# Performance work log

Hardware: AMD Instinct MI355X
Metric: run time of the kernel (lower is better)

## Reference

```python
import jax, jax.numpy as jnp
import numpy as np

D_MODEL = 1024
N_HEADS = 16
D_HEAD = 64
INIT_RANGE = 0.02
IGNORE = -100000.0


def setup_inputs() -> dict:
    key = jax.random.key(0)
    ks = jax.random.split(key, 5)
    x = jax.random.normal(ks[0], (2, 2048, D_MODEL), dtype=jnp.float32)
    W_Q = jax.random.normal(ks[1], (N_HEADS, D_MODEL, D_HEAD), dtype=jnp.float32) * INIT_RANGE
    W_K = jax.random.normal(ks[2], (N_HEADS, D_MODEL, D_HEAD), dtype=jnp.float32) * INIT_RANGE
    W_V = jax.random.normal(ks[3], (N_HEADS, D_MODEL, D_HEAD), dtype=jnp.float32) * INIT_RANGE
    W_O = jax.random.normal(ks[4], (N_HEADS, D_HEAD, D_MODEL), dtype=jnp.float32) * INIT_RANGE
    b_Q = jnp.zeros((N_HEADS, D_HEAD), dtype=jnp.float32)
    b_K = jnp.zeros((N_HEADS, D_HEAD), dtype=jnp.float32)
    b_V = jnp.zeros((N_HEADS, D_HEAD), dtype=jnp.float32)
    b_O = jnp.zeros((D_MODEL,), dtype=jnp.float32)
    return {"normalized_resid_pre": x, "W_Q": W_Q, "W_K": W_K, "W_V": W_V,
            "W_O": W_O, "b_Q": b_Q, "b_K": b_K, "b_V": b_V, "b_O": b_O}


def reference(normalized_resid_pre, W_Q, W_K, W_V, W_O, b_Q, b_K, b_V, b_O):
    x = normalized_resid_pre  # [b, s, d_model]
    q = jnp.einsum('bsd,hde->bshe', x, W_Q) + b_Q  # [b, s, h, d_head]
    k = jnp.einsum('bsd,hde->bshe', x, W_K) + b_K
    v = jnp.einsum('bsd,hde->bshe', x, W_V) + b_V
    scores = jnp.einsum('bqhe,bkhe->bhqk', q, k) / jnp.sqrt(jnp.float32(D_HEAD))
    s = x.shape[1]
    causal = jnp.arange(s)[:, None] >= jnp.arange(s)[None, :]  # [q, k]
    scores = jnp.where(causal, scores, jnp.float32(IGNORE))
    pattern = jax.nn.softmax(scores, axis=-1)  # [b, h, q, k]
    z = jnp.einsum('bkhe,bhqk->bqhe', v, pattern)
    out = jnp.einsum('bqhe,hed->bqd', z, W_O) + b_O
    return out
```

## Files before the change

kernel.cpp:

```cpp
#include <hip/hip_runtime.h>

#define SEQ 2048
#define BATCH 2
#define DM 1024
#define NH 16
#define DH 64

typedef __bf16 bf16;
typedef __bf16 bf16x8 __attribute__((ext_vector_type(8)));
typedef __bf16 bf16x4 __attribute__((ext_vector_type(4)));
typedef float f32x4 __attribute__((ext_vector_type(4)));

#define MFMA16(a, b, c) __builtin_amdgcn_mfma_f32_16x16x32_bf16((a), (b), (c), 0, 0, 0)

#if __has_builtin(__builtin_amdgcn_exp2f)
#define EXP2(x) __builtin_amdgcn_exp2f(x)
#else
#define EXP2(x) exp2f(x)
#endif

#define QSCALE 0.18033688f

typedef __attribute__((address_space(3))) void lds_void;
typedef __attribute__((address_space(1))) void glb_void;
__device__ __forceinline__ void gld16(void* lds, const void* g) {
    __builtin_amdgcn_global_load_lds((const glb_void*)g, (lds_void*)lds, 16, 0, 0);
}

__global__ __launch_bounds__(256) void k_prep(const float* __restrict__ x,
                                              const float* __restrict__ WQ,
                                              const float* __restrict__ WK,
                                              const float* __restrict__ WV,
                                              const float* __restrict__ WO,
                                              bf16* __restrict__ xb,
                                              bf16* __restrict__ wT,
                                              bf16* __restrict__ woT) {
    int bx = blockIdx.x;
    int t = threadIdx.x;
    if (bx < 2048) {
        int g = bx * 256 + t;
        const float4* x4 = (const float4*)x;
        float4 a = x4[2 * g];
        float4 b = x4[2 * g + 1];
        bf16x8 o;
        o[0] = (bf16)a.x; o[1] = (bf16)a.y; o[2] = (bf16)a.z; o[3] = (bf16)a.w;
        o[4] = (bf16)b.x; o[5] = (bf16)b.y; o[6] = (bf16)b.z; o[7] = (bf16)b.w;
        *(bf16x8*)(xb + 8 * g) = o;
        return;
    }
    __shared__ bf16 T[64 * 65];
    if (bx < 2816) {
        int id = bx - 2048;
        int kt = id & 15, ph = id >> 4;
        int p = ph >> 4, h = ph & 15;
        const float* Wp = (p == 0) ? WQ : (p == 1) ? WK : WV;
        const float* src = Wp + ((size_t)h * DM + (size_t)kt * 64) * DH;
        for (int i = 0; i < 4; i++) {
            int c = t + 256 * i;
            int r = c >> 4;
            int col = (c & 15) * 4;
            float4 v = *(const float4*)&src[r * 64 + col];
            T[(col + 0) * 65 + r] = (bf16)v.x;
            T[(col + 1) * 65 + r] = (bf16)v.y;
            T[(col + 2) * 65 + r] = (bf16)v.z;
            T[(col + 3) * 65 + r] = (bf16)v.w;
        }
        __syncthreads();
        bf16* dst = wT + (size_t)ph * 64 * DM + (size_t)kt * 64;
        for (int i = 0; i < 2; i++) {
            int c = t + 256 * i;
            int e = c >> 3;
            int k0 = (c & 7) * 8;
            bf16x8 o;
            for (int j = 0; j < 8; j++) o[j] = T[e * 65 + k0 + j];
            *(bf16x8*)&dst[(size_t)e * DM + k0] = o;
        }
    } else {
        int id = bx - 2816;
        int ht = id & 15, dt = id >> 4;
        for (int i = 0; i < 4; i++) {
            int c = t + 256 * i;
            int r = c >> 4;
            int col = (c & 15) * 4;
            float4 v = *(const float4*)&WO[((size_t)(ht * 64 + r)) * DM + dt * 64 + col];
            T[(col + 0) * 65 + r] = (bf16)v.x;
            T[(col + 1) * 65 + r] = (bf16)v.y;
            T[(col + 2) * 65 + r] = (bf16)v.z;
            T[(col + 3) * 65 + r] = (bf16)v.w;
        }
        __syncthreads();
        for (int i = 0; i < 2; i++) {
            int c = t + 256 * i;
            int d = c >> 3;
            int h0 = (c & 7) * 8;
            bf16x8 o;
            for (int j = 0; j < 8; j++) o[j] = T[d * 65 + h0 + j];
            *(bf16x8*)&woT[((size_t)(dt * 64 + d)) * DM + ht * 64 + h0] = o;
        }
    }
}

__global__ __launch_bounds__(512, 2) void k_qkv(const bf16* __restrict__ xb,
                                                const bf16* __restrict__ wT,
                                                const float* __restrict__ bQ,
                                                const float* __restrict__ bK,
                                                const float* __restrict__ bV,
                                                bf16* __restrict__ Qb,
                                                bf16* __restrict__ Kb,
                                                bf16* __restrict__ VTf) {
    int mt = blockIdx.x, nt = blockIdx.y;
    __shared__ __align__(16) char sm[114688];
    int t = threadIdx.x;
    int lane = t & 63, w = t >> 6;
    int l15 = lane & 15, quad = lane >> 4;
    int wr = w >> 2, wc = w & 3;
    int m0 = mt * 256;
    int n0 = nt * 192;

    int P0 = t * 16;
    int L0 = P0 ^ (((P0 >> 7) & 3) << 4);
    int row0 = L0 >> 6, kc0 = (L0 >> 4) & 3;
    int P1 = 8192 + t * 16;
    int L1 = P1 ^ (((P1 >> 7) & 3) << 4);
    int row1 = L1 >> 6, kc1 = (L1 >> 4) & 3;
    const bf16* gA0 = xb + (size_t)(m0 + row0) * DM + kc0 * 8;
    const bf16* gA1 = xb + (size_t)(m0 + row1) * DM + kc1 * 8;
    const bf16* gB0 = wT + (size_t)(n0 + row0) * DM + kc0 * 8;
    const bf16* gB1 = wT + (size_t)(n0 + row1) * DM + kc1 * 8;

    auto stage = [&](int ts, bool bsel) {
        char* sb = sm + (ts & 3) * 28672;
        int ko = ts * 32;
        if (!bsel) {
            gld16(sb + w * 1024, gA0 + ko);
            gld16(sb + 8192 + w * 1024, gA1 + ko);
        } else {
            gld16(sb + 16384 + w * 1024, gB0 + ko);
            if (w < 4) gld16(sb + 16384 + 8192 + w * 1024, gB1 + ko);
        }
    };

    int aoff[8], boff[3];
#pragma unroll
    for (int mi = 0; mi < 8; mi++) {
        int row = wr * 128 + mi * 16 + l15;
        aoff[mi] = row * 64 + ((quad ^ ((row >> 1) & 3)) << 4);
    }
#pragma unroll
    for (int ni = 0; ni < 3; ni++) {
        int row = wc * 48 + ni * 16 + l15;
        boff[ni] = 16384 + row * 64 + ((quad ^ ((row >> 1) & 3)) << 4);
    }

    const f32x4 z4 = {0.f, 0.f, 0.f, 0.f};
    f32x4 acc[8][3];
#pragma unroll
    for (int mi = 0; mi < 8; mi++)
#pragma unroll
        for (int ni = 0; ni < 3; ni++) acc[mi][ni] = z4;

    auto kstep = [&](int tt, bool st) {
        const char* sb = sm + (tt & 3) * 28672;
        bf16x8 bfr[3], afr[4];
#pragma unroll
        for (int ni = 0; ni < 3; ni++) bfr[ni] = *(const bf16x8*)(sb + boff[ni]);
#pragma unroll
        for (int mi = 0; mi < 4; mi++) afr[mi] = *(const bf16x8*)(sb + aoff[mi]);
        if (st) stage(tt + 3, false);
        __builtin_amdgcn_s_setprio(1);
#pragma unroll
        for (int mi = 0; mi < 4; mi++)
#pragma unroll
            for (int ni = 0; ni < 3; ni++)
                acc[mi][ni] = MFMA16(afr[mi], bfr[ni], acc[mi][ni]);
        __builtin_amdgcn_s_setprio(0);
        bf16x8 afr2[4];
#pragma unroll
        for (int mi = 0; mi < 4; mi++) afr2[mi] = *(const bf16x8*)(sb + aoff[4 + mi]);
        if (st) stage(tt + 3, true);
        __builtin_amdgcn_s_setprio(1);
#pragma unroll
        for (int mi = 0; mi < 4; mi++)
#pragma unroll
            for (int ni = 0; ni < 3; ni++)
                acc[4 + mi][ni] = MFMA16(afr2[mi], bfr[ni], acc[4 + mi][ni]);
        __builtin_amdgcn_s_setprio(0);
    };

#define QKV_WAIT(N03, N47)                                              \
    do {                                                                \
        if (w < 4) asm volatile("s_waitcnt vmcnt(" #N03 ")" ::: "memory"); \
        else       asm volatile("s_waitcnt vmcnt(" #N47 ")" ::: "memory"); \
        asm volatile("s_barrier" ::: "memory");                         \
        __builtin_amdgcn_sched_barrier(0);                              \
    } while (0)

    stage(0, false); stage(0, true);
    stage(1, false); stage(1, true);
    stage(2, false); stage(2, true);

#pragma unroll 1
    for (int tt = 0; tt < 29; tt++) {
        QKV_WAIT(8, 6);
        kstep(tt, true);
    }
    QKV_WAIT(8, 6);
    kstep(29, false);
    QKV_WAIT(4, 3);
    kstep(30, false);
    QKV_WAIT(0, 0);
    kstep(31, false);
#undef QKV_WAIT

    int b = mt >> 3;
#pragma unroll
    for (int ni = 0; ni < 3; ni++) {
        int he3 = n0 + wc * 48 + ni * 16 + l15;
        int p = he3 >> 10;
        int he = he3 & 1023;
        int h = he >> 6, e = he & 63;
        if (p < 2) {
            const float* bias = (p == 0) ? bQ : bK;
            bf16* dst = (p == 0) ? Qb : Kb;
            float scale = (p == 0) ? QSCALE : 1.0f;
            float bia = bias[he];
            size_t rb = (size_t)(b * NH + h) * SEQ * DH + e;
#pragma unroll
            for (int mi = 0; mi < 8; mi++)
#pragma unroll
                for (int r = 0; r < 4; r++) {
                    int s = ((m0 + wr * 128 + mi * 16 + quad * 4 + r) & 2047);
                    dst[rb + (size_t)s * DH] = (bf16)((acc[mi][ni][r] + bia) * scale);
                }
        } else {
            int no = (he3 >> 4) & 3;
            float bia = bV[he];
#pragma unroll
            for (int mi = 0; mi < 8; mi++) {
                int kvl = (mt & 7) * 256 + wr * 128 + mi * 16;
                int kt = kvl >> 7;
                int f = (mi >> 1) * 4 + no;
                size_t base = (((size_t)(b * NH + h) * 16 + kt) * 16 + f) * 512
                              + (size_t)((quad << 4) | l15) * 8 + (mi & 1) * 4;
                bf16x4 o;
#pragma unroll
                for (int r = 0; r < 4; r++) o[r] = (bf16)(acc[mi][ni][r] + bia);
                *(bf16x4*)&VTf[base] = o;
            }
        }
    }
}

__global__ __launch_bounds__(512, 4) void k_attn(const bf16* __restrict__ Qb,
                                                 const bf16* __restrict__ Kb,
                                                 const bf16* __restrict__ VTf,
                                                 bf16* __restrict__ Zb) {
    int bh = blockIdx.x;
    int y = blockIdx.y;
    int qt = (y < 8) ? y : 23 - y;
    int h = bh & 15, b = bh >> 4;
    __shared__ __align__(16) bf16 Ks[2][16 * 512];
    __shared__ __align__(16) bf16 Vs[16 * 512];
    int t = threadIdx.x;
    int lane = t & 63, w = t >> 6;
    int l15 = lane & 15, quad = lane >> 4;

    const bf16* qbase = Qb + (size_t)bh * SEQ * DH;
    const bf16* kbase = Kb + (size_t)bh * SEQ * DH;
    const bf16* vfrag = VTf + (size_t)bh * 16 * 8192;

    int qr0 = qt * 128 + w * 16;
    bf16x8 aq[2];
    for (int ks = 0; ks < 2; ks++)
        aq[ks] = *(const bf16x8*)&qbase[(size_t)(qr0 + l15) * DH + ks * 32 + quad * 8];

    auto stageK = [&](int buf, int kt) {
        for (int i = 0; i < 2; i++) {
            int f = w * 2 + i;
            int ks = f >> 3, ni = f & 7;
            gld16(&Ks[buf][f * 512],
                  kbase + (size_t)(kt * 128 + ni * 16 + l15) * DH + ks * 32 + quad * 8);
        }
    };
    auto stageV = [&](int kt) {
        const bf16* vt = vfrag + (size_t)kt * 8192;
        for (int i = 0; i < 2; i++) {
            int f = w * 2 + i;
            gld16(&Vs[f * 512], vt + f * 512 + lane * 8);
        }
    };

    const bf16 one = (bf16)1.0f;
    const bf16x8 ones = {one, one, one, one, one, one, one, one};
    const f32x4 z4 = {0.f, 0.f, 0.f, 0.f};
    f32x4 acco[4], accd;
    for (int no = 0; no < 4; no++) acco[no] = z4;
    accd = z4;

    stageK(0, 0);

    for (int kt = 0; kt <= qt; kt++) {
        int buf = kt & 1;
        asm volatile("s_waitcnt vmcnt(0)\n\ts_barrier" ::: "memory");
        __builtin_amdgcn_sched_barrier(0);
        stageV(kt);
        if (kt < qt) stageK(buf ^ 1, kt + 1);
        const bf16* Kbuf = Ks[buf];

        f32x4 accs[8];
        for (int ni = 0; ni < 8; ni++) accs[ni] = z4;
        __builtin_amdgcn_s_setprio(1);
        for (int ks = 0; ks < 2; ks++)
            for (int ni = 0; ni < 8; ni++) {
                bf16x8 ak = *(const bf16x8*)&Kbuf[(ks * 8 + ni) * 512 + lane * 8];
                accs[ni] = MFMA16(ak, aq[ks], accs[ni]);
            }
        __builtin_amdgcn_s_setprio(0);

        if (kt == qt) {
            int ql = w * 16 + l15;
            for (int ni = 0; ni < 8; ni++) {
                int kvl = ni * 16 + quad * 4;
                for (int r = 0; r < 4; r++)
                    if (kvl + r > ql) accs[ni][r] = -1e30f;
            }
        }

        bf16x4 pt[8];
        for (int ni = 0; ni < 8; ni++)
            for (int r = 0; r < 4; r++)
                pt[ni][r] = (bf16)EXP2(accs[ni][r]);

        if (kt < qt) {
            asm volatile("s_waitcnt vmcnt(2)\n\ts_barrier" ::: "memory");
        } else {
            asm volatile("s_waitcnt vmcnt(0)\n\ts_barrier" ::: "memory");
        }
        __builtin_amdgcn_sched_barrier(0);

        __builtin_amdgcn_s_setprio(1);
        for (int p4 = 0; p4 < 4; p4++) {
            bf16x8 ap;
            for (int j = 0; j < 4; j++) {
                ap[j] = pt[2 * p4][j];
                ap[4 + j] = pt[2 * p4 + 1][j];
            }
            accd = MFMA16(ap, ones, accd);
            for (int no = 0; no < 4; no++) {
                bf16x8 bv = *(const bf16x8*)&Vs[(p4 * 4 + no) * 512 + lane * 8];
                acco[no] = MFMA16(ap, bv, acco[no]);
            }
        }
        __builtin_amdgcn_s_setprio(0);
    }

    for (int r = 0; r < 4; r++) {
        float inv = 1.0f / accd[r];
        int q = qr0 + quad * 4 + r;
        size_t rowbase = ((size_t)b * SEQ + q) * DM + h * DH;
        for (int no = 0; no < 4; no++)
            Zb[rowbase + no * 16 + l15] = (bf16)(acco[no][r] * inv);
    }
}

__global__ __launch_bounds__(256, 2) void k_out(const bf16* __restrict__ Zb,
                                                const bf16* __restrict__ woT,
                                                const float* __restrict__ bO,
                                                float* __restrict__ out) {
    int mt = blockIdx.x, nt = blockIdx.y;
    __shared__ __align__(16) char sm[65536];
    int t = threadIdx.x;
    int lane = t & 63, w = t >> 6;
    int l15 = lane & 15, quad = lane >> 4;
    int wr = w >> 1, wc = w & 1;
    int m0 = mt * 128, n0 = nt * 128;

    int P0 = t * 16;
    int L0 = P0 ^ (((P0 >> 7) & 3) << 4);
    int row0 = L0 >> 6, kc0 = (L0 >> 4) & 3;
    int P1 = 4096 + t * 16;
    int L1 = P1 ^ (((P1 >> 7) & 3) << 4);
    int row1 = L1 >> 6, kc1 = (L1 >> 4) & 3;
    const bf16* gA0 = Zb + (size_t)(m0 + row0) * DM + kc0 * 8;
    const bf16* gA1 = Zb + (size_t)(m0 + row1) * DM + kc1 * 8;
    const bf16* gB0 = woT + (size_t)(n0 + row0) * DM + kc0 * 8;
    const bf16* gB1 = woT + (size_t)(n0 + row1) * DM + kc1 * 8;

    auto stage = [&](int ts) {
        char* sb = sm + (ts & 3) * 16384;
        int ko = ts * 32;
        gld16(sb + w * 1024, gA0 + ko);
        gld16(sb + 4096 + w * 1024, gA1 + ko);
        gld16(sb + 8192 + w * 1024, gB0 + ko);
        gld16(sb + 8192 + 4096 + w * 1024, gB1 + ko);
    };

    int aoff[4], boff[4];
#pragma unroll
    for (int mi = 0; mi < 4; mi++) {
        int row = wr * 64 + mi * 16 + l15;
        aoff[mi] = row * 64 + ((quad ^ ((row >> 1) & 3)) << 4);
    }
#pragma unroll
    for (int ni = 0; ni < 4; ni++) {
        int row = wc * 64 + ni * 16 + l15;
        boff[ni] = 8192 + row * 64 + ((quad ^ ((row >> 1) & 3)) << 4);
    }

    const f32x4 z4 = {0.f, 0.f, 0.f, 0.f};
    f32x4 acc[4][4];
#pragma unroll
    for (int mi = 0; mi < 4; mi++)
#pragma unroll
        for (int ni = 0; ni < 4; ni++) acc[mi][ni] = z4;

    auto kstep = [&](int tt, bool st) {
        const char* sb = sm + (tt & 3) * 16384;
        bf16x8 bfr[4], afr[4];
#pragma unroll
        for (int ni = 0; ni < 4; ni++) bfr[ni] = *(const bf16x8*)(sb + boff[ni]);
#pragma unroll
        for (int mi = 0; mi < 4; mi++) afr[mi] = *(const bf16x8*)(sb + aoff[mi]);
        if (st) stage(tt + 3);
        __builtin_amdgcn_s_setprio(1);
#pragma unroll
        for (int mi = 0; mi < 4; mi++)
#pragma unroll
            for (int ni = 0; ni < 4; ni++)
                acc[mi][ni] = MFMA16(afr[mi], bfr[ni], acc[mi][ni]);
        __builtin_amdgcn_s_setprio(0);
    };

    stage(0); stage(1); stage(2);

#pragma unroll 1
    for (int tt = 0; tt < 29; tt++) {
        asm volatile("s_waitcnt vmcnt(8)\n\ts_barrier" ::: "memory");
        __builtin_amdgcn_sched_barrier(0);
        kstep(tt, true);
    }
    asm volatile("s_waitcnt vmcnt(8)\n\ts_barrier" ::: "memory");
    __builtin_amdgcn_sched_barrier(0);
    kstep(29, false);
    asm volatile("s_waitcnt vmcnt(4)\n\ts_barrier" ::: "memory");
    __builtin_amdgcn_sched_barrier(0);
    kstep(30, false);
    asm volatile("s_waitcnt vmcnt(0)\n\ts_barrier" ::: "memory");
    __builtin_amdgcn_sched_barrier(0);
    kstep(31, false);

#pragma unroll
    for (int ni = 0; ni < 4; ni++) {
        int d = n0 + wc * 64 + ni * 16 + l15;
        float bia = bO[d];
#pragma unroll
        for (int mi = 0; mi < 4; mi++)
#pragma unroll
            for (int r = 0; r < 4; r++) {
                int s = m0 + wr * 64 + mi * 16 + quad * 4 + r;
                out[(size_t)s * DM + d] = acc[mi][ni][r] + bia;
            }
    }
}

extern "C" void kernel_launch(void* const* d_in, const int* in_sizes, int n_in,
                              void* d_out, int out_size, void* d_ws, size_t ws_size,
                              hipStream_t stream) {
    const float* x  = (const float*)d_in[0];
    const float* WQ = (const float*)d_in[1];
    const float* WK = (const float*)d_in[2];
    const float* WV = (const float*)d_in[3];
    const float* WO = (const float*)d_in[4];
    const float* bQ = (const float*)d_in[5];
    const float* bK = (const float*)d_in[6];
    const float* bV = (const float*)d_in[7];
    const float* bO = (const float*)d_in[8];
    float* out = (float*)d_out;

    char* w = (char*)d_ws;
    bf16* xb    = (bf16*)(w + 0);
    bf16* wqkvT = (bf16*)(w + (8u << 20));
    bf16* woT   = (bf16*)(w + (14u << 20));
    bf16* Qb    = (bf16*)(w + (16u << 20));
    bf16* Kb    = (bf16*)(w + (24u << 20));
    bf16* VTf   = (bf16*)(w + (32u << 20));
    bf16* Zb    = (bf16*)(w + (40u << 20));

    k_prep<<<3072, 256, 0, stream>>>(x, WQ, WK, WV, WO, xb, wqkvT, woT);
    k_qkv<<<dim3(16, 16), 512, 0, stream>>>(xb, wqkvT, bQ, bK, bV, Qb, Kb, VTf);
    k_attn<<<dim3(32, 16), 512, 0, stream>>>(Qb, Kb, VTf, Zb);
    k_out<<<dim3(32, 8), 256, 0, stream>>>(Zb, woT, bO, out);
}
```

Measured before the change: 162.0 us.

## Split long causal attention tiles across two blocks with atomic combine

Query tiles 8-15 of the causal attention kernel are now split along the key dimension into two halves, each handled by its own block. The grid grows from 16 to 24 rows per head. Each half writes unnormalized partial outputs and denominators to a float workspace and bumps an atomic counter. The second block to finish sums the halves and writes the normalized result. The aim is to balance work and shorten the critical path of the longest tiles, at the cost of extra global traffic, a memset, and fence/atomic synchronization.

```diff
diff --git a/kernel.cpp b/kernel.cpp
--- a/kernel.cpp
+++ b/kernel.cpp
@@ -254,16 +254,34 @@
 __global__ __launch_bounds__(512, 4) void k_attn(const bf16* __restrict__ Qb,
                                                  const bf16* __restrict__ Kb,
                                                  const bf16* __restrict__ VTf,
-                                                 bf16* __restrict__ Zb) {
+                                                 bf16* __restrict__ Zb,
+                                                 float* __restrict__ Pacc,
+                                                 int* __restrict__ Tk) {
     int bh = blockIdx.x;
     int y = blockIdx.y;
-    int qt = (y < 8) ? y : 23 - y;
     int h = bh & 15, b = bh >> 4;
     __shared__ __align__(16) bf16 Ks[2][16 * 512];
     __shared__ __align__(16) bf16 Vs[16 * 512];
+    __shared__ int sOld;
     int t = threadIdx.x;
     int lane = t & 63, w = t >> 6;
     int l15 = lane & 15, quad = lane >> 4;
+
+    int qt, kt0, kt1, seg;
+    if (y < 8) {
+        qt = y; kt0 = 0; kt1 = qt; seg = -1;
+    } else {
+        const int qtA[8] = {15, 13, 13, 11, 11, 9, 9, 8};
+        const int sgA[8] = {0, 0, 1, 0, 1, 0, 1, 0};
+        const int qtB[8] = {15, 14, 14, 12, 12, 10, 10, 8};
+        const int sgB[8] = {1, 1, 0, 1, 0, 1, 0, 1};
+        int g = (y - 8) & 7;
+        if (y < 16) { qt = qtA[g]; seg = sgA[g]; }
+        else        { qt = qtB[g]; seg = sgB[g]; }
+        int hh = (qt + 1) >> 1;
+        kt0 = seg ? hh : 0;
+        kt1 = seg ? qt : hh - 1;
+    }
 
     const bf16* qbase = Qb + (size_t)bh * SEQ * DH;
     const bf16* kbase = Kb + (size_t)bh * SEQ * DH;
@@ -297,14 +315,14 @@
     for (int no = 0; no < 4; no++) acco[no] = z4;
     accd = z4;
 
-    stageK(0, 0);
-
-    for (int kt = 0; kt <= qt; kt++) {
-        int buf = kt & 1;
+    stageK(0, kt0);
+
+    for (int kt = kt0; kt <= kt1; kt++) {
+        int buf = (kt - kt0) & 1;
         asm volatile("s_waitcnt vmcnt(0)\n\ts_barrier" ::: "memory");
         __builtin_amdgcn_sched_barrier(0);
         stageV(kt);
-        if (kt < qt) stageK(buf ^ 1, kt + 1);
+        if (kt < kt1) stageK(buf ^ 1, kt + 1);
         const bf16* Kbuf = Ks[buf];
 
         f32x4 accs[8];
@@ -331,7 +349,7 @@
             for (int r = 0; r < 4; r++)
                 pt[ni][r] = (bf16)EXP2(accs[ni][r]);
 
-        if (kt < qt) {
+        if (kt < kt1) {
             asm volatile("s_waitcnt vmcnt(2)\n\ts_barrier" ::: "memory");
         } else {
             asm volatile("s_waitcnt vmcnt(0)\n\ts_barrier" ::: "memory");
@@ -354,12 +372,47 @@
         __builtin_amdgcn_s_setprio(0);
     }
 
+    if (seg < 0) {
+        for (int r = 0; r < 4; r++) {
+            float inv = 1.0f / accd[r];
+            int q = qr0 + quad * 4 + r;
+            size_t rowbase = ((size_t)b * SEQ + q) * DM + h * DH;
+            for (int no = 0; no < 4; no++)
+                Zb[rowbase + no * 16 + l15] = (bf16)(acco[no][r] * inv);
+        }
+        return;
+    }
+
+    int qt8 = qt - 8;
+    int pairIdx = bh * 8 + qt8;
+    size_t s0 = (size_t)(pairIdx * 2) * 8448;
+    float* Om = Pacc + s0 + (size_t)seg * 8448;
+    float* Dm = Om + 8192;
+    int qrow = w * 16 + quad * 4;
     for (int r = 0; r < 4; r++) {
-        float inv = 1.0f / accd[r];
-        int q = qr0 + quad * 4 + r;
-        size_t rowbase = ((size_t)b * SEQ + q) * DM + h * DH;
         for (int no = 0; no < 4; no++)
-            Zb[rowbase + no * 16 + l15] = (bf16)(acco[no][r] * inv);
+            Om[(qrow + r) * 64 + no * 16 + l15] = acco[no][r];
+        if (l15 == 0) Dm[qrow + r] = accd[r];
+    }
+    __syncthreads();
+    if (t == 0) {
+        __threadfence();
+        sOld = atomicAdd(&Tk[pairIdx], 1);
+    }
+    __syncthreads();
+    if (sOld == 1) {
+        __threadfence();
+        const float* O0 = Pacc + s0;
+        const float* D0 = O0 + 8192;
+        const float* O1 = O0 + 8448;
+        const float* D1 = O1 + 8192;
+        int row = t >> 2;
+        int c0 = (t & 3) * 16;
+        float inv = 1.0f / (D0[row] + D1[row]);
+        int q = qt * 128 + row;
+        bf16* dst = &Zb[((size_t)b * SEQ + q) * DM + h * DH + c0];
+        for (int j = 0; j < 16; j++)
+            dst[j] = (bf16)((O0[row * 64 + c0 + j] + O1[row * 64 + c0 + j]) * inv);
     }
 }
 
@@ -485,9 +538,12 @@
     bf16* Kb    = (bf16*)(w + (24u << 20));
     bf16* VTf   = (bf16*)(w + (32u << 20));
     bf16* Zb    = (bf16*)(w + (40u << 20));
-
+    float* Pacc = (float*)(w + (48u << 20));
+    int*  Tk    = (int*)(w + (66u << 20));
+
+    hipMemsetAsync(Tk, 0, 32 * 8 * sizeof(int), stream);
     k_prep<<<3072, 256, 0, stream>>>(x, WQ, WK, WV, WO, xb, wqkvT, woT);
     k_qkv<<<dim3(16, 16), 512, 0, stream>>>(xb, wqkvT, bQ, bK, bV, Qb, Kb, VTf);
-    k_attn<<<dim3(32, 16), 512, 0, stream>>>(Qb, Kb, VTf, Zb);
+    k_attn<<<dim3(32, 24), 512, 0, stream>>>(Qb, Kb, VTf, Zb, Pacc, Tk);
     k_out<<<dim3(32, 8), 256, 0, stream>>>(Zb, woT, bO, out);
 }
```

Measured after the change: 235.2 us. 45.2% more time.
